# Optimization experiments

Measured on AMD Instinct MI355X. Metric: run time of the kernel, lower is better.

## Reference

```python
import jax, jax.numpy as jnp
import numpy as np

SS, D, V = 64, 256, 10000
B, S = 16, 512


def setup_inputs() -> dict:
    key = jax.random.key(0)
    ks = jax.random.split(key, 7)
    scale = lambda fan_in: 1.0 / np.sqrt(fan_in)
    return {
        "x": jax.random.normal(ks[0], (B, S, D), dtype=jnp.float32),
        # nn.Linear(D, 4*ss): weight [4ss, D], bias [4ss]
        "Wxs_w": jax.random.uniform(ks[1], (4 * SS, D), jnp.float32, -scale(D), scale(D)),
        "Wxs_b": jax.random.uniform(ks[2], (4 * SS,), jnp.float32, -scale(D), scale(D)),
        # nn.Linear(ss, 4*ss)
        "Wss_w": jax.random.uniform(ks[3], (4 * SS, SS), jnp.float32, -scale(SS), scale(SS)),
        "Wss_b": jax.random.uniform(ks[4], (4 * SS,), jnp.float32, -scale(SS), scale(SS)),
        # nn.Linear(ss, V)
        "Wsy_w": jax.random.uniform(ks[5], (V, SS), jnp.float32, -scale(SS), scale(SS)),
        "Wsy_b": jax.random.uniform(ks[6], (V,), jnp.float32, -scale(SS), scale(SS)),
    }


def reference(x, Wxs_w, Wxs_b, Wss_w, Wss_b, Wsy_w, Wsy_b):
    b, s, _ = x.shape
    ss = Wss_w.shape[1]
    # Precompute input projections for all timesteps: [s, b, 4ss]
    xproj = jnp.einsum("bsd,kd->sbk", x, Wxs_w) + Wxs_b

    def step(carry, xp_t):
        h, c = carry
        comb = xp_t + h @ Wss_w.T + Wss_b  # [b, 4ss]
        f, i, g, o = jnp.split(comb, 4, axis=-1)
        f = jax.nn.sigmoid(f)
        i = jax.nn.sigmoid(i)
        o = jax.nn.sigmoid(o)
        g = jnp.tanh(g)
        c = c * f + i * g
        h = o * c  # NOTE: original code omits tanh(c) here; stay faithful
        return (h, c), h

    h0 = jnp.zeros((b, ss), dtype=x.dtype)
    c0 = jnp.zeros((b, ss), dtype=x.dtype)
    _, hs = jax.lax.scan(step, (h0, c0), xproj)  # hs: [s, b, ss]
    # Per-step vocab projection == batched projection of stacked hidden states
    y = jnp.einsum("sbh,vh->bsv", hs, Wsy_w) + Wsy_b  # [b, s, V]
    return y
```

## Files before the change

kernel.cpp:

```cpp
#include <hip/hip_runtime.h>

typedef unsigned short u16;
typedef unsigned int u32;

using short8 = __attribute__((ext_vector_type(8))) short;
using f32x4  = __attribute__((ext_vector_type(4))) float;
using f32x2  = __attribute__((ext_vector_type(2))) float;

#define SSEQ 512
#define BB   16
#define DD   256
#define G4   256
#define SSZ  64
#define VV   10000
#define VPAD 10112
#define MALL 8192

#define OFF_XHI   0u
#define OFF_XLO   4194304u
#define OFF_WHI   8388608u
#define OFF_WLO   8519680u
#define OFF_WSY   8650752u
#define OFF_XPROJ 9945088u
#define OFF_HS    18333696u

__device__ __forceinline__ u16 f2bf(float f) {
  u32 u = __float_as_uint(f);
  u32 r = (u + 0x7fffu + ((u >> 16) & 1u)) >> 16;
  return (u16)r;
}
__device__ __forceinline__ float bf2f(u16 h) {
  return __uint_as_float(((u32)h) << 16);
}
__device__ __forceinline__ f32x2 pkfma(f32x2 a, f32x2 b, f32x2 c) {
  asm("v_pk_fma_f32 %0, %1, %2, %0" : "+v"(c) : "v"(a), "v"(b));
  return c;
}
template <int CTRL>
__device__ __forceinline__ float qadd(float x) {
  int pv = __builtin_amdgcn_update_dpp(0, __float_as_int(x), CTRL, 0xf, 0xf, true);
  return x + __int_as_float(pv);
}
template <int CTRL>
__device__ __forceinline__ float qbcast(float x) {
  int pv = __builtin_amdgcn_update_dpp(0, __float_as_int(x), CTRL, 0xf, 0xf, true);
  return __int_as_float(pv);
}

#define NX 2097152
#define NW 65536
#define NP 647168
__global__ void k0_convert(const float* __restrict__ x, const float* __restrict__ Wxs,
                           const float* __restrict__ Wsy,
                           u16* __restrict__ xhi, u16* __restrict__ xlo,
                           u16* __restrict__ whi, u16* __restrict__ wlo,
                           u16* __restrict__ wsyb) {
  int i = blockIdx.x * 256 + threadIdx.x;
  if (i < NX) {
    float v = x[i]; u16 h = f2bf(v);
    xhi[i] = h; xlo[i] = f2bf(v - bf2f(h));
  } else if (i < NX + NW) {
    int j = i - NX;
    float v = Wxs[j]; u16 h = f2bf(v);
    whi[j] = h; wlo[j] = f2bf(v - bf2f(h));
  } else if (i < NX + NW + NP) {
    int j = i - NX - NW;
    wsyb[j] = (j < VV * SSZ) ? f2bf(Wsy[j]) : (u16)0;
  }
}

__global__ __launch_bounds__(256) void k1_xproj(
    const u16* __restrict__ xhi, const u16* __restrict__ xlo,
    const u16* __restrict__ whi, const u16* __restrict__ wlo,
    const float* __restrict__ bias, float* __restrict__ xproj) {
  int bid = blockIdx.x;
  int mb = bid >> 1, nb = bid & 1;
  int tid = threadIdx.x, l = tid & 63, wid = tid >> 6;
  int wm = wid >> 1, wv = wid & 1;
  int m0 = mb * 128 + wm * 64, n0 = nb * 128 + wv * 64;
  int lr = l & 15, lg = l >> 4;

  f32x4 acc[4][4];
#pragma unroll
  for (int a = 0; a < 4; a++)
#pragma unroll
    for (int bq = 0; bq < 4; bq++) acc[a][bq] = (f32x4){0.f, 0.f, 0.f, 0.f};

#pragma unroll
  for (int p = 0; p < 3; p++) {
    const u16* A = (p == 1) ? xlo : xhi;
    const u16* B = (p == 2) ? wlo : whi;
#pragma unroll
    for (int ks = 0; ks < 8; ks++) {
      short8 af[4], bf_[4];
#pragma unroll
      for (int fm = 0; fm < 4; fm++)
        af[fm] = *(const short8*)(A + (size_t)(m0 + fm * 16 + lr) * 256 + ks * 32 + lg * 8);
#pragma unroll
      for (int fv = 0; fv < 4; fv++)
        bf_[fv] = *(const short8*)(B + (size_t)(n0 + fv * 16 + lr) * 256 + ks * 32 + lg * 8);
#pragma unroll
      for (int fm = 0; fm < 4; fm++)
#pragma unroll
        for (int fv = 0; fv < 4; fv++)
          acc[fm][fv] = __builtin_amdgcn_mfma_f32_16x16x32_bf16(af[fm], bf_[fv], acc[fm][fv], 0, 0, 0);
    }
  }
#pragma unroll
  for (int fv = 0; fv < 4; fv++) {
    int j = n0 + fv * 16 + lr;
    float bj = bias[j];
#pragma unroll
    for (int fm = 0; fm < 4; fm++)
#pragma unroll
      for (int r = 0; r < 4; r++) {
        int m = m0 + fm * 16 + lg * 4 + r;
        xproj[(size_t)m * 256 + j] = acc[fm][fv][r] + bj;
      }
  }
}

__global__ __launch_bounds__(256, 1) void k2_scan(
    const float* __restrict__ xproj, const float* __restrict__ Wss,
    const float* __restrict__ Wssb, u16* __restrict__ hsb) {
  __shared__ float hbuf[2][64];
  __shared__ u16 hstage[SSEQ][64];

  int b = blockIdx.x, tid = threadIdx.x;
  int w = tid >> 6, l = tid & 63;
  int oo = l >> 2, ks = l & 3;
  int jj = w * 16 + oo;
  int ks16 = ks * 16;

  f32x2 wr[32];
#pragma unroll
  for (int g = 0; g < 4; g++) {
    const f32x2* pw = (const f32x2*)(Wss + (size_t)(g * 64 + jj) * 64 + ks16);
#pragma unroll
    for (int q = 0; q < 8; q++) wr[g * 8 + q] = pw[q];
  }
  float mybias = Wssb[ks * 64 + jj];

  float kk = (ks == 2) ? 2.885390082f : -1.442695041f;
  float Ac = (ks == 2) ? 1.f : 0.f;
  float Bc = (ks == 2) ? -2.f : 1.f;

  const float* xqp = xproj + (size_t)b * SSEQ * 256 + ks * 64 + jj;
  float xs0 = xqp[0 * 256];
  float xs1 = xqp[1 * 256];
  float xs2 = xqp[2 * 256];
  float xs3 = xqp[3 * 256];

  if (tid < 128) ((float*)hbuf)[tid] = 0.f;
  __syncthreads();

  float c = 0.f;

#define STEP(T, XS, RB, WB) { \
    f32x4 h4[4]; \
    const f32x4* hb = (const f32x4*)&hbuf[RB][ks16]; \
    h4[0] = hb[0]; h4[1] = hb[1]; h4[2] = hb[2]; h4[3] = hb[3]; \
    float p[4]; \
    _Pragma("unroll") \
    for (int g = 0; g < 4; g++) { \
      f32x2 a0 = (f32x2){0.f, 0.f}, a1 = (f32x2){0.f, 0.f}; \
      _Pragma("unroll") \
      for (int q = 0; q < 4; q++) { \
        f32x2 hA = (f32x2){h4[q][0], h4[q][1]}; \
        f32x2 hB = (f32x2){h4[q][2], h4[q][3]}; \
        a0 = pkfma(hA, wr[g * 8 + 2 * q], a0); \
        a1 = pkfma(hB, wr[g * 8 + 2 * q + 1], a1); \
      } \
      p[g] = (a0[0] + a0[1]) + (a1[0] + a1[1]); \
    } \
    _Pragma("unroll") \
    for (int g = 0; g < 4; g++) p[g] = qadd<0x4E>(qadd<0xB1>(p[g])); \
    float myp = (ks == 1) ? p[1] : p[0]; \
    myp = (ks == 2) ? p[2] : myp; \
    myp = (ks == 3) ? p[3] : myp; \
    float aa = myp + XS + mybias; \
    if ((T) + 4 < SSEQ) XS = xqp[(size_t)((T) + 4) * 256]; \
    float z = exp2f(kk * aa); \
    float act = fmaf(Bc, __builtin_amdgcn_rcpf(z + 1.f), Ac); \
    float fg = qbcast<0x00>(act); \
    float ig = qbcast<0x55>(act); \
    float gg = qbcast<0xAA>(act); \
    float og = qbcast<0xFF>(act); \
    c = fmaf(c, fg, ig * gg); \
    float hn = og * c;   \
    if (ks == 0) { \
      hbuf[WB][jj] = hn; \
      hstage[T][jj] = f2bf(hn); \
    } \
    asm volatile("s_waitcnt lgkmcnt(0)\n\ts_barrier" ::: "memory"); \
  }

  for (int t = 0; t < SSEQ; t += 4) {
    STEP(t + 0, xs0, 1, 0)
    STEP(t + 1, xs1, 0, 1)
    STEP(t + 2, xs2, 1, 0)
    STEP(t + 3, xs3, 0, 1)
  }
#undef STEP

  __syncthreads();
  const uint4* src = (const uint4*)hstage;
  uint4* dst = (uint4*)(hsb + (size_t)b * SSEQ * 64);
#pragma unroll
  for (int i = 0; i < 16; i++) dst[tid + 256 * i] = src[tid + 256 * i];
}

__global__ __launch_bounds__(256) void k3_y(
    const u16* __restrict__ hsb, const u16* __restrict__ wsyb,
    const float* __restrict__ bias, float* __restrict__ y) {
  int bid = blockIdx.x;
  int mb = bid / 79, vb = bid - mb * 79;
  int tid = threadIdx.x, l = tid & 63, wid = tid >> 6;
  int wm = wid >> 1, wv = wid & 1;
  int m0 = mb * 128 + wm * 64, v0 = vb * 128 + wv * 64;
  int lr = l & 15, lg = l >> 4;

  f32x4 acc[4][4];
#pragma unroll
  for (int a = 0; a < 4; a++)
#pragma unroll
    for (int bq = 0; bq < 4; bq++) acc[a][bq] = (f32x4){0.f, 0.f, 0.f, 0.f};

#pragma unroll
  for (int ks = 0; ks < 2; ks++) {
    short8 af[4], bf_[4];
#pragma unroll
    for (int fm = 0; fm < 4; fm++)
      af[fm] = *(const short8*)(hsb + (size_t)(m0 + fm * 16 + lr) * 64 + ks * 32 + lg * 8);
#pragma unroll
    for (int fv = 0; fv < 4; fv++)
      bf_[fv] = *(const short8*)(wsyb + (size_t)(v0 + fv * 16 + lr) * 64 + ks * 32 + lg * 8);
#pragma unroll
    for (int fv = 0; fv < 4; fv++)
#pragma unroll
      for (int fm = 0; fm < 4; fm++)
        acc[fv][fm] = __builtin_amdgcn_mfma_f32_16x16x32_bf16(bf_[fv], af[fm], acc[fv][fm], 0, 0, 0);
  }

#pragma unroll
  for (int fv = 0; fv < 4; fv++) {
    int vb4 = v0 + fv * 16 + lg * 4;
    bool ok = (vb4 + 3) < VV;
    float4 bv = ok ? *(const float4*)(bias + vb4) : float4{0.f, 0.f, 0.f, 0.f};
#pragma unroll
    for (int fm = 0; fm < 4; fm++) {
      int m = m0 + fm * 16 + lr;
      if (ok) {
        float4 o;
        o.x = acc[fv][fm][0] + bv.x;
        o.y = acc[fv][fm][1] + bv.y;
        o.z = acc[fv][fm][2] + bv.z;
        o.w = acc[fv][fm][3] + bv.w;
        *(float4*)(y + (size_t)m * (size_t)VV + vb4) = o;
      }
    }
  }
}

extern "C" void kernel_launch(void* const* d_in, const int* in_sizes, int n_in,
                              void* d_out, int out_size, void* d_ws, size_t ws_size,
                              hipStream_t stream) {
  const float* x     = (const float*)d_in[0];
  const float* Wxs_w = (const float*)d_in[1];
  const float* Wxs_b = (const float*)d_in[2];
  const float* Wss_w = (const float*)d_in[3];
  const float* Wss_b = (const float*)d_in[4];
  const float* Wsy_w = (const float*)d_in[5];
  const float* Wsy_b = (const float*)d_in[6];
  float* y = (float*)d_out;
  char* ws = (char*)d_ws;

  u16*   xhi   = (u16*)(ws + OFF_XHI);
  u16*   xlo   = (u16*)(ws + OFF_XLO);
  u16*   whi   = (u16*)(ws + OFF_WHI);
  u16*   wlo   = (u16*)(ws + OFF_WLO);
  u16*   wsyb  = (u16*)(ws + OFF_WSY);
  float* xproj = (float*)(ws + OFF_XPROJ);
  u16*   hsb   = (u16*)(ws + OFF_HS);

  k0_convert<<<(NX + NW + NP) / 256, 256, 0, stream>>>(x, Wxs_w, Wsy_w, xhi, xlo, whi, wlo, wsyb);
  k1_xproj<<<128, 256, 0, stream>>>(xhi, xlo, whi, wlo, Wxs_b, xproj);
  k2_scan<<<16, 256, 0, stream>>>(xproj, Wss_w, Wss_b, hsb);
  k3_y<<<64 * 79, 256, 0, stream>>>(hsb, wsyb, Wsy_b, y);
}
```

Before: 281.0 us.

## Fuse scan and vocab projection with progress flags to overlap GEMM with recurrence

The recurrence kernel and the vocab projection GEMM become one persistent kernel of 256 blocks. Sixteen blocks run the per-batch LSTM scan, write bf16 hidden states straight to global memory, and publish an atomic progress counter every 32 steps. The other 240 blocks spin on those counters and compute 128-row output tiles as soon as the rows they need are ready. The intent is to hide the large output-write GEMM behind the latency-bound serial scan, at the cost of relying on all blocks being co-resident and adding spin-waits and extra global stores inside the scan loop.

```diff
diff --git a/kernel.cpp b/kernel.cpp
--- a/kernel.cpp
+++ b/kernel.cpp
@@ -23,6 +23,7 @@
 #define OFF_WSY   8650752u
 #define OFF_XPROJ 9945088u
 #define OFF_HS    18333696u
+#define OFF_PROG  19382272u
 
 __device__ __forceinline__ u16 f2bf(float f) {
   u32 u = __float_as_uint(f);
@@ -54,7 +55,7 @@
                            const float* __restrict__ Wsy,
                            u16* __restrict__ xhi, u16* __restrict__ xlo,
                            u16* __restrict__ whi, u16* __restrict__ wlo,
-                           u16* __restrict__ wsyb) {
+                           u16* __restrict__ wsyb, int* __restrict__ prog) {
   int i = blockIdx.x * 256 + threadIdx.x;
   if (i < NX) {
     float v = x[i]; u16 h = f2bf(v);
@@ -66,6 +67,10 @@
   } else if (i < NX + NW + NP) {
     int j = i - NX - NW;
     wsyb[j] = (j < VV * SSZ) ? f2bf(Wsy[j]) : (u16)0;
+  } else {
+    int j = i - NX - NW - NP;
+    if (j < BB)
+      __hip_atomic_store(prog + j, 0, __ATOMIC_RELEASE, __HIP_MEMORY_SCOPE_AGENT);
   }
 }
 
@@ -120,41 +125,46 @@
   }
 }
 
-__global__ __launch_bounds__(256, 1) void k2_scan(
+__global__ __launch_bounds__(256, 1) void k23_fused(
     const float* __restrict__ xproj, const float* __restrict__ Wss,
-    const float* __restrict__ Wssb, u16* __restrict__ hsb) {
+    const float* __restrict__ Wssb, u16* __restrict__ hsb,
+    const u16* __restrict__ wsyb, const float* __restrict__ ybias,
+    float* __restrict__ y, int* __restrict__ prog) {
   __shared__ float hbuf[2][64];
-  __shared__ u16 hstage[SSEQ][64];
-
-  int b = blockIdx.x, tid = threadIdx.x;
-  int w = tid >> 6, l = tid & 63;
-  int oo = l >> 2, ks = l & 3;
-  int jj = w * 16 + oo;
-  int ks16 = ks * 16;
-
-  f32x2 wr[32];
-#pragma unroll
-  for (int g = 0; g < 4; g++) {
-    const f32x2* pw = (const f32x2*)(Wss + (size_t)(g * 64 + jj) * 64 + ks16);
-#pragma unroll
-    for (int q = 0; q < 8; q++) wr[g * 8 + q] = pw[q];
-  }
-  float mybias = Wssb[ks * 64 + jj];
-
-  float kk = (ks == 2) ? 2.885390082f : -1.442695041f;
-  float Ac = (ks == 2) ? 1.f : 0.f;
-  float Bc = (ks == 2) ? -2.f : 1.f;
-
-  const float* xqp = xproj + (size_t)b * SSEQ * 256 + ks * 64 + jj;
-  float xs0 = xqp[0 * 256];
-  float xs1 = xqp[1 * 256];
-  float xs2 = xqp[2 * 256];
-  float xs3 = xqp[3 * 256];
-
-  if (tid < 128) ((float*)hbuf)[tid] = 0.f;
-  __syncthreads();
-
-  float c = 0.f;
+  int bid = blockIdx.x, tid = threadIdx.x;
+
+  if (bid < BB) {
+    int b = bid;
+    int w = tid >> 6, l = tid & 63;
+    int oo = l >> 2, ks = l & 3;
+    int jj = w * 16 + oo;
+    int ks16 = ks * 16;
+
+    f32x2 wr[32];
+#pragma unroll
+    for (int g = 0; g < 4; g++) {
+      const f32x2* pw = (const f32x2*)(Wss + (size_t)(g * 64 + jj) * 64 + ks16);
+#pragma unroll
+      for (int q = 0; q < 8; q++) wr[g * 8 + q] = pw[q];
+    }
+    float mybias = Wssb[ks * 64 + jj];
+
+    float kk = (ks == 2) ? 2.885390082f : -1.442695041f;
+    float Ac = (ks == 2) ? 1.f : 0.f;
+    float Bc = (ks == 2) ? -2.f : 1.f;
+
+    const float* xqp = xproj + (size_t)b * SSEQ * 256 + ks * 64 + jj;
+    float xs0 = xqp[0 * 256];
+    float xs1 = xqp[1 * 256];
+    float xs2 = xqp[2 * 256];
+    float xs3 = xqp[3 * 256];
+
+    u16* hout = hsb + (size_t)b * SSEQ * 64 + jj;
+
+    if (tid < 128) ((float*)hbuf)[tid] = 0.f;
+    __syncthreads();
+
+    float c = 0.f;
 
 #define STEP(T, XS, RB, WB) { \
     f32x4 h4[4]; \
@@ -171,7 +181,8 @@
         a0 = pkfma(hA, wr[g * 8 + 2 * q], a0); \
         a1 = pkfma(hB, wr[g * 8 + 2 * q + 1], a1); \
       } \
-      p[g] = (a0[0] + a0[1]) + (a1[0] + a1[1]); \
+      f32x2 ps = a0 + a1; \
+      p[g] = ps[0] + ps[1]; \
     } \
     _Pragma("unroll") \
     for (int g = 0; g < 4; g++) p[g] = qadd<0x4E>(qadd<0xB1>(p[g])); \
@@ -190,73 +201,84 @@
     float hn = og * c;   \
     if (ks == 0) { \
       hbuf[WB][jj] = hn; \
-      hstage[T][jj] = f2bf(hn); \
+      __builtin_nontemporal_store(f2bf(hn), hout + (size_t)(T) * 64); \
     } \
     asm volatile("s_waitcnt lgkmcnt(0)\n\ts_barrier" ::: "memory"); \
   }
 
-  for (int t = 0; t < SSEQ; t += 4) {
-    STEP(t + 0, xs0, 1, 0)
-    STEP(t + 1, xs1, 0, 1)
-    STEP(t + 2, xs2, 1, 0)
-    STEP(t + 3, xs3, 0, 1)
-  }
+    for (int t = 0; t < SSEQ; t += 32) {
+#pragma unroll
+      for (int tq = 0; tq < 32; tq += 4) {
+        STEP(t + tq + 0, xs0, 1, 0)
+        STEP(t + tq + 1, xs1, 0, 1)
+        STEP(t + tq + 2, xs2, 1, 0)
+        STEP(t + tq + 3, xs3, 0, 1)
+      }
+      asm volatile("s_waitcnt vmcnt(0)" ::: "memory");
+      __syncthreads();
+      if (tid == 0)
+        __hip_atomic_store(prog + b, t + 32, __ATOMIC_RELEASE, __HIP_MEMORY_SCOPE_AGENT);
+    }
 #undef STEP
-
-  __syncthreads();
-  const uint4* src = (const uint4*)hstage;
-  uint4* dst = (uint4*)(hsb + (size_t)b * SSEQ * 64);
-#pragma unroll
-  for (int i = 0; i < 16; i++) dst[tid + 256 * i] = src[tid + 256 * i];
-}
-
-__global__ __launch_bounds__(256) void k3_y(
-    const u16* __restrict__ hsb, const u16* __restrict__ wsyb,
-    const float* __restrict__ bias, float* __restrict__ y) {
-  int bid = blockIdx.x;
-  int mb = bid / 79, vb = bid - mb * 79;
-  int tid = threadIdx.x, l = tid & 63, wid = tid >> 6;
-  int wm = wid >> 1, wv = wid & 1;
-  int m0 = mb * 128 + wm * 64, v0 = vb * 128 + wv * 64;
-  int lr = l & 15, lg = l >> 4;
-
-  f32x4 acc[4][4];
-#pragma unroll
-  for (int a = 0; a < 4; a++)
-#pragma unroll
-    for (int bq = 0; bq < 4; bq++) acc[a][bq] = (f32x4){0.f, 0.f, 0.f, 0.f};
-
-#pragma unroll
-  for (int ks = 0; ks < 2; ks++) {
-    short8 af[4], bf_[4];
-#pragma unroll
-    for (int fm = 0; fm < 4; fm++)
-      af[fm] = *(const short8*)(hsb + (size_t)(m0 + fm * 16 + lr) * 64 + ks * 32 + lg * 8);
-#pragma unroll
-    for (int fv = 0; fv < 4; fv++)
-      bf_[fv] = *(const short8*)(wsyb + (size_t)(v0 + fv * 16 + lr) * 64 + ks * 32 + lg * 8);
-#pragma unroll
-    for (int fv = 0; fv < 4; fv++)
-#pragma unroll
-      for (int fm = 0; fm < 4; fm++)
-        acc[fv][fm] = __builtin_amdgcn_mfma_f32_16x16x32_bf16(bf_[fv], af[fm], acc[fv][fm], 0, 0, 0);
-  }
-
-#pragma unroll
-  for (int fv = 0; fv < 4; fv++) {
-    int vb4 = v0 + fv * 16 + lg * 4;
-    bool ok = (vb4 + 3) < VV;
-    float4 bv = ok ? *(const float4*)(bias + vb4) : float4{0.f, 0.f, 0.f, 0.f};
-#pragma unroll
-    for (int fm = 0; fm < 4; fm++) {
-      int m = m0 + fm * 16 + lr;
-      if (ok) {
-        float4 o;
-        o.x = acc[fv][fm][0] + bv.x;
-        o.y = acc[fv][fm][1] + bv.y;
-        o.z = acc[fv][fm][2] + bv.z;
-        o.w = acc[fv][fm][3] + bv.w;
-        *(float4*)(y + (size_t)m * (size_t)VV + vb4) = o;
+  } else {
+    int gb = bid - BB;
+    int l = tid & 63, wid = tid >> 6;
+    int wm = wid >> 1, wv = wid & 1;
+    int lr = l & 15, lg = l >> 4;
+
+    for (int idx = gb; idx < 4 * BB * 79; idx += 256 - BB) {
+      int tb = idx / (BB * 79);
+      int rem = idx - tb * BB * 79;
+      int b = rem / 79;
+      int vb = rem - b * 79;
+      int need = tb * 128 + 128;
+
+      while (__hip_atomic_load(prog + b, __ATOMIC_RELAXED, __HIP_MEMORY_SCOPE_AGENT) < need)
+        __builtin_amdgcn_s_sleep(32);
+      __builtin_amdgcn_fence(__ATOMIC_ACQUIRE, "agent");
+
+      int m0 = b * SSEQ + tb * 128 + wm * 64;
+      int v0 = vb * 128 + wv * 64;
+
+      f32x4 acc[4][4];
+#pragma unroll
+      for (int a = 0; a < 4; a++)
+#pragma unroll
+        for (int bq = 0; bq < 4; bq++) acc[a][bq] = (f32x4){0.f, 0.f, 0.f, 0.f};
+
+#pragma unroll
+      for (int ks = 0; ks < 2; ks++) {
+        short8 af[4], bf_[4];
+#pragma unroll
+        for (int fm = 0; fm < 4; fm++)
+          af[fm] = *(const short8*)(hsb + (size_t)(m0 + fm * 16 + lr) * 64 + ks * 32 + lg * 8);
+#pragma unroll
+        for (int fv = 0; fv < 4; fv++)
+          bf_[fv] = *(const short8*)(wsyb + (size_t)(v0 + fv * 16 + lr) * 64 + ks * 32 + lg * 8);
+#pragma unroll
+        for (int fv = 0; fv < 4; fv++)
+#pragma unroll
+          for (int fm = 0; fm < 4; fm++)
+            acc[fv][fm] = __builtin_amdgcn_mfma_f32_16x16x32_bf16(bf_[fv], af[fm], acc[fv][fm], 0, 0, 0);
+      }
+
+#pragma unroll
+      for (int fv = 0; fv < 4; fv++) {
+        int vb4 = v0 + fv * 16 + lg * 4;
+        bool ok = (vb4 + 3) < VV;
+        float4 bv = ok ? *(const float4*)(ybias + vb4) : float4{0.f, 0.f, 0.f, 0.f};
+#pragma unroll
+        for (int fm = 0; fm < 4; fm++) {
+          int m = m0 + fm * 16 + lr;
+          if (ok) {
+            float4 o;
+            o.x = acc[fv][fm][0] + bv.x;
+            o.y = acc[fv][fm][1] + bv.y;
+            o.z = acc[fv][fm][2] + bv.z;
+            o.w = acc[fv][fm][3] + bv.w;
+            *(float4*)(y + (size_t)m * (size_t)VV + vb4) = o;
+          }
+        }
       }
     }
   }
@@ -282,9 +304,10 @@
   u16*   wsyb  = (u16*)(ws + OFF_WSY);
   float* xproj = (float*)(ws + OFF_XPROJ);
   u16*   hsb   = (u16*)(ws + OFF_HS);
-
-  k0_convert<<<(NX + NW + NP) / 256, 256, 0, stream>>>(x, Wxs_w, Wsy_w, xhi, xlo, whi, wlo, wsyb);
+  int*   prog  = (int*)(ws + OFF_PROG);
+
+  k0_convert<<<(NX + NW + NP) / 256 + 1, 256, 0, stream>>>(
+      x, Wxs_w, Wsy_w, xhi, xlo, whi, wlo, wsyb, prog);
   k1_xproj<<<128, 256, 0, stream>>>(xhi, xlo, whi, wlo, Wxs_b, xproj);
-  k2_scan<<<16, 256, 0, stream>>>(xproj, Wss_w, Wss_b, hsb);
-  k3_y<<<64 * 79, 256, 0, stream>>>(hsb, wsyb, Wsy_b, y);
-}
+  k23_fused<<<256, 256, 0, stream>>>(xproj, Wss_w, Wss_b, hsb, wsyb, Wsy_b, y, prog);
+}
```

After: 290.1 us. +3.3%, slower.
